# Kernel optimization log

Measured on AMD Instinct MI355X. Metric: run time of the kernel, lower is better.

## Reference

```python
import jax, jax.numpy as jnp
import numpy as np
from math import sqrt

D_MODEL = 768
N_HEADS = 12
D_K = 64
D_V = 64
LN_EPS = 1e-5
NEG = -1e9


def layer_norm(x, g, b):
    mu = jnp.mean(x, axis=-1, keepdims=True)
    var = jnp.mean((x - mu) ** 2, axis=-1, keepdims=True)
    return (x - mu) * jax.lax.rsqrt(var + LN_EPS) * g + b


def setup_inputs() -> dict:
    key = jax.random.key(0)
    ks = jax.random.split(key, 8)
    B, S = 4, 1024
    pro1 = jax.random.normal(ks[0], (B, S, D_MODEL), dtype=jnp.float32)
    pro2 = jax.random.normal(ks[1], (B, S, D_MODEL), dtype=jnp.float32)
    # attn_mask is [B, H, S2, S1]; transpose(2,3) masks scores [B,H,S1,S2]
    mask1_2 = jax.random.bernoulli(ks[2], 0.3, (B, N_HEADS, S, S))
    sc = 1.0 / np.sqrt(D_MODEL)
    W_Q = jax.random.normal(ks[3], (D_MODEL, D_K * N_HEADS), dtype=jnp.float32) * sc
    W_K = jax.random.normal(ks[4], (D_MODEL, D_K * N_HEADS), dtype=jnp.float32) * sc
    fc1 = jax.random.normal(ks[5], (D_V * N_HEADS, D_MODEL), dtype=jnp.float32) * sc
    g1 = jnp.ones((D_MODEL,), jnp.float32)
    b1 = jnp.zeros((D_MODEL,), jnp.float32)
    g2 = jnp.ones((D_MODEL,), jnp.float32)
    b2 = jnp.zeros((D_MODEL,), jnp.float32)
    return {"pro1": pro1, "pro2": pro2, "mask1_2": mask1_2,
            "W_Q": W_Q, "W_K": W_K, "fc1": fc1,
            "g1": g1, "b1": b1, "g2": g2, "b2": b2}


def reference(pro1, pro2, mask1_2, W_Q, W_K, fc1, g1, b1, g2, b2):
    B, S1, _ = pro1.shape
    S2 = pro2.shape[1]
    # project and split heads: [B, H, S, d_k]
    Q = (pro1 @ W_Q).reshape(B, S1, N_HEADS, D_K).transpose(0, 2, 1, 3)
    K = (pro2 @ W_K).reshape(B, S2, N_HEADS, D_K).transpose(0, 2, 1, 3)
    scores = jnp.einsum('bhsd,bhtd->bhst', Q, K) / sqrt(D_K)  # [B,H,S1,S2]
    mask = jnp.swapaxes(mask1_2, 2, 3)  # attn_mask.transpose(2,3)
    scores = jnp.where(mask, NEG, scores)
    attn1 = jax.nn.softmax(scores, axis=-1)                  # over S2
    attn2 = jax.nn.softmax(jnp.swapaxes(scores, -1, -2), axis=-1)  # over S1
    ctx1 = jnp.einsum('bhst,bhtd->bhsd', attn1, K)  # [B,H,S1,d_k]
    ctx2 = jnp.einsum('bhts,bhsd->bhtd', attn2, Q)  # [B,H,S2,d_k]
    c1 = ctx1.transpose(0, 2, 1, 3).reshape(B, S1, N_HEADS * D_V)
    c2 = ctx2.transpose(0, 2, 1, 3).reshape(B, S2, N_HEADS * D_V)
    # NOTE: original applies fc1 to BOTH branches (fc2 is dead code)
    o1 = layer_norm(c1 @ fc1, g1, b1)
    o2 = layer_norm(c2 @ fc1, g2, b2)
    return (o1, o2)
```

## Files before the change

### kernel.cpp

```cpp
#include <hip/hip_runtime.h>
#include <hip/hip_bf16.h>
#include <stdint.h>

#define S 1024
#define DMODEL 768
#define NH 12
#define DK 64
#define BB 4
#define BH 48
#define M4 4096

typedef __attribute__((ext_vector_type(8))) short bf16x8;
typedef __attribute__((ext_vector_type(4))) float f32x4;
typedef __attribute__((ext_vector_type(4))) _Float16 f16x4;
typedef __attribute__((ext_vector_type(8))) _Float16 f16x8;

static __device__ __forceinline__ unsigned short f2bf(float f) {
  unsigned int u = __float_as_uint(f);
  unsigned int r = u + 0x7FFFu + ((u >> 16) & 1u);
  return (unsigned short)(r >> 16);
}
static __device__ __forceinline__ bf16x8 ldfrag(const unsigned short* p) {
  uint4 q = *reinterpret_cast<const uint4*>(p);
  return __builtin_bit_cast(bf16x8, q);
}
static __device__ __forceinline__ f16x8 ldfragh(const unsigned short* p) {
  uint4 q = *reinterpret_cast<const uint4*>(p);
  return __builtin_bit_cast(f16x8, q);
}
static __device__ __forceinline__ unsigned short h2u(_Float16 h) {
  return __builtin_bit_cast(unsigned short, h);
}
static __device__ __forceinline__ void gl2lds16(const unsigned short* g, unsigned short* l) {
  __builtin_amdgcn_global_load_lds(
      (const __attribute__((address_space(1))) unsigned int*)g,
      (__attribute__((address_space(3))) unsigned int*)l, 16, 0, 0);
}

__global__ __launch_bounds__(256) void k_convert(const float* __restrict__ in,
                                                 unsigned short* __restrict__ out, int n4) {
  int i = blockIdx.x * 256 + threadIdx.x;
  if (i < n4) {
    float4 v = reinterpret_cast<const float4*>(in)[i];
    ushort4 o;
    o.x = f2bf(v.x); o.y = f2bf(v.y); o.z = f2bf(v.z); o.w = f2bf(v.w);
    reinterpret_cast<ushort4*>(out)[i] = o;
  }
}

__global__ __launch_bounds__(256) void k_transpose(const float* w0, const float* w1, const float* w2,
                                                   unsigned short* o0, unsigned short* o1, unsigned short* o2) {
  const float* in = blockIdx.z == 0 ? w0 : (blockIdx.z == 1 ? w1 : w2);
  unsigned short* out = blockIdx.z == 0 ? o0 : (blockIdx.z == 1 ? o1 : o2);
  __shared__ float tile[32][33];
  int n0 = blockIdx.x * 32, k0 = blockIdx.y * 32;
  int tid = threadIdx.x;
  int r = tid >> 3, c = (tid & 7) * 4;
  float4 v = *reinterpret_cast<const float4*>(in + (size_t)(k0 + r) * DMODEL + n0 + c);
  tile[r][c] = v.x; tile[r][c + 1] = v.y; tile[r][c + 2] = v.z; tile[r][c + 3] = v.w;
  __syncthreads();
  ushort4 o;
  o.x = f2bf(tile[c + 0][r]);
  o.y = f2bf(tile[c + 1][r]);
  o.z = f2bf(tile[c + 2][r]);
  o.w = f2bf(tile[c + 3][r]);
  *reinterpret_cast<ushort4*>(out + (size_t)(n0 + r) * DMODEL + k0 + c) = o;
}

__global__ __launch_bounds__(256) void k_pack(const int* __restrict__ mask,
                                              unsigned int* __restrict__ mp2) {
  int bh = blockIdx.y;
  int w = threadIdx.x >> 6, lane = threadIdx.x & 63;
  int tile = blockIdx.x * 4 + w;
  int ti = tile >> 4, tj = tile & 15;
  int t0 = ti * 64, s0 = tj * 64;
  const int* mb = mask + (size_t)bh * S * S;
  unsigned long long rowword = 0;
#pragma unroll 8
  for (int r = 0; r < 64; ++r) {
    int v = mb[(size_t)(t0 + r) * S + s0 + lane];
    unsigned long long b = __ballot(v != 0);
    if (lane == r) rowword = b;
  }
  unsigned int* p2 = mp2 + (size_t)bh * 32 * S;
  p2[((s0 >> 5) + 0) * S + t0 + lane] = (unsigned int)rowword;
  p2[((s0 >> 5) + 1) * S + t0 + lane] = (unsigned int)(rowword >> 32);
}

__global__ __launch_bounds__(256, 3) void k_gemm(
    int mode,
    const unsigned short* __restrict__ A0, const unsigned short* __restrict__ A1,
    const unsigned short* __restrict__ Bt0, const unsigned short* __restrict__ Bt1,
    unsigned short* __restrict__ oQ0, unsigned short* __restrict__ oQ1,
    unsigned short* __restrict__ oT0, unsigned short* __restrict__ oT1,
    float* __restrict__ oF0, float* __restrict__ oF1) {
  const unsigned short* A = blockIdx.z ? A1 : A0;
  const unsigned short* Bt = blockIdx.z ? Bt1 : Bt0;
  __shared__ __align__(16) unsigned short As[128 * 64];
  __shared__ __align__(16) unsigned short Bs[128 * 64];
  int tid = threadIdx.x;
  int m0 = blockIdx.x * 128, n0 = blockIdx.y * 128;
  int w = tid >> 6, lane = tid & 63, lane15 = lane & 15, quad = lane >> 4;
  int row0 = (w >> 1) * 64, col0 = (w & 1) * 64;
  f32x4 acc[4][4] = {};

  const unsigned short* gA[4];
  const unsigned short* gB[4];
  unsigned short* lA[4];
  unsigned short* lB[4];
  {
    int lr = lane >> 3;
    int ch = lane & 7;
#pragma unroll
    for (int i = 0; i < 4; ++i) {
      int r = w * 32 + i * 8 + lr;
      int cs = ((ch ^ (r & 7)) * 8);
      gA[i] = A + (size_t)(m0 + r) * DMODEL + cs;
      gB[i] = Bt + (size_t)(n0 + r) * DMODEL + cs;
      lA[i] = &As[(w * 32 + i * 8) * 64];
      lB[i] = &Bs[(w * 32 + i * 8) * 64];
    }
  }
  int l7 = lane15 & 7;
#pragma unroll
  for (int i = 0; i < 4; ++i) { gl2lds16(gA[i], lA[i]); gl2lds16(gB[i], lB[i]); }

  for (int kc = 0; kc < 12; ++kc) {
    __syncthreads();
#pragma unroll
    for (int ks = 0; ks < 2; ++ks) {
      int co = (((ks * 4 + quad) ^ l7) * 8);
      bf16x8 a[4], b[4];
#pragma unroll
      for (int i = 0; i < 4; ++i) a[i] = ldfrag(&As[(row0 + i * 16 + lane15) * 64 + co]);
#pragma unroll
      for (int j = 0; j < 4; ++j) b[j] = ldfrag(&Bs[(col0 + j * 16 + lane15) * 64 + co]);
#pragma unroll
      for (int i = 0; i < 4; ++i)
#pragma unroll
        for (int j = 0; j < 4; ++j)
          acc[i][j] = __builtin_amdgcn_mfma_f32_16x16x32_bf16(a[i], b[j], acc[i][j], 0, 0, 0);
    }
    __syncthreads();
    if (kc < 11) {
      int ko = (kc + 1) * 64;
#pragma unroll
      for (int i = 0; i < 4; ++i) { gl2lds16(gA[i] + ko, lA[i]); gl2lds16(gB[i] + ko, lB[i]); }
    }
  }

  if (mode == 0) {
    unsigned short* out = blockIdx.z ? oQ1 : oQ0;
    unsigned short* outT = blockIdx.z ? oT1 : oT0;
    f16x4 iden;
#pragma unroll
    for (int i = 0; i < 4; ++i) iden[i] = (_Float16)((quad * 4 + i) == lane15 ? 1.0f : 0.0f);
    f32x4 zero4 = {};
#pragma unroll
    for (int i = 0; i < 4; ++i)
#pragma unroll
      for (int j = 0; j < 4; ++j) {
        f16x4 cf;
#pragma unroll
        for (int reg = 0; reg < 4; ++reg) cf[reg] = (_Float16)acc[i][j][reg];
        f32x4 tq = __builtin_amdgcn_mfma_f32_16x16x16f16(cf, iden, zero4, 0, 0, 0);
        {
          int m = m0 + row0 + i * 16 + lane15;
          int n = n0 + col0 + j * 16 + quad * 4;
          int b = m >> 10, s = m & 1023, h = n >> 6, d = n & 63;
          ushort4 o;
          o.x = h2u((_Float16)tq[0]); o.y = h2u((_Float16)tq[1]);
          o.z = h2u((_Float16)tq[2]); o.w = h2u((_Float16)tq[3]);
          *reinterpret_cast<ushort4*>(&out[(((size_t)(b * NH + h)) * S + s) * DK + d]) = o;
        }
        {
          int n = n0 + col0 + j * 16 + lane15;
          int m = m0 + row0 + i * 16 + quad * 4;
          int b = m >> 10, s = m & 1023, h = n >> 6, d = n & 63;
          ushort4 o;
          o.x = h2u((_Float16)acc[i][j][0]); o.y = h2u((_Float16)acc[i][j][1]);
          o.z = h2u((_Float16)acc[i][j][2]); o.w = h2u((_Float16)acc[i][j][3]);
          *reinterpret_cast<ushort4*>(&outT[(((size_t)(b * NH + h)) * DK + d) * S + s]) = o;
        }
      }
  } else {
    float* out = blockIdx.z ? oF1 : oF0;
#pragma unroll
    for (int i = 0; i < 4; ++i)
#pragma unroll
      for (int j = 0; j < 4; ++j)
#pragma unroll
        for (int reg = 0; reg < 4; ++reg) {
          int m = m0 + row0 + i * 16 + quad * 4 + reg;
          int n = n0 + col0 + j * 16 + lane15;
          out[(size_t)m * DMODEL + n] = acc[i][j][reg];
        }
  }
}

__global__ __launch_bounds__(256, 3) void k_attn(
    const unsigned short* __restrict__ Qb, const unsigned short* __restrict__ Kb,
    const unsigned short* __restrict__ QT, const unsigned short* __restrict__ KT,
    const unsigned int* __restrict__ mp2,
    unsigned short* __restrict__ c1, unsigned short* __restrict__ c2) {
  int bh = blockIdx.y, path = blockIdx.z;
  int s0b = blockIdx.x * 128;
  const unsigned short* X = path ? Kb : Qb;
  const unsigned short* Y = path ? Qb : Kb;
  const unsigned short* YT = path ? QT : KT;
  unsigned short* outc = path ? c2 : c1;

  __shared__ __align__(16) unsigned short YS[64 * 72];
  __shared__ __align__(16) unsigned short YTS[64 * 72];
  __shared__ unsigned int MWS[256];

  const unsigned short* Xb = X + (size_t)bh * S * DK;
  const unsigned short* Yb = Y + (size_t)bh * S * DK;
  const unsigned short* YTb = YT + (size_t)bh * DK * S;
  const unsigned int* mbg = mp2 + (size_t)bh * 32 * S;

  int tid = threadIdx.x;
  int w = tid >> 6, lane = tid & 63, lane15 = lane & 15, quad = lane >> 4;
  int s0w = s0b + w * 32;

  f16x8 xf[2][2];
#pragma unroll
  for (int rg = 0; rg < 2; ++rg) {
    xf[rg][0] = ldfragh(Xb + (size_t)(s0w + rg * 16 + lane15) * DK + quad * 8);
    xf[rg][1] = ldfragh(Xb + (size_t)(s0w + rg * 16 + lane15) * DK + 32 + quad * 8);
  }

  int sr4 = tid >> 2, sc4 = (tid & 3) * 16;
  const unsigned short* gY = Yb + (size_t)sr4 * DK + sc4;
  const unsigned short* gYT = YTb + (size_t)sr4 * S + sc4;
  uint4 y0 = *reinterpret_cast<const uint4*>(gY);
  uint4 y1 = *reinterpret_cast<const uint4*>(gY + 8);
  uint4 t0 = *reinterpret_cast<const uint4*>(gYT);
  uint4 t1 = *reinterpret_cast<const uint4*>(gYT + 8);
  int mws_idx = (path == 0) ? ((tid & 63) * 4 + (tid >> 6)) : ((tid & 127) * 2 + (tid >> 7));
  unsigned int mwv = (path == 0)
      ? mbg[((size_t)((s0b >> 5) + (tid >> 6))) * S + (tid & 63)]
      : mbg[((size_t)(tid >> 7)) * S + s0b + (tid & 127)];

  f32x4 outa[2][4] = {};
  float lsum[2] = {0.f, 0.f};

  for (int jc = 0; jc < 16; ++jc) {
    __syncthreads();
    *reinterpret_cast<uint4*>(&YS[sr4 * 72 + sc4]) = y0;
    *reinterpret_cast<uint4*>(&YS[sr4 * 72 + sc4 + 8]) = y1;
    *reinterpret_cast<uint4*>(&YTS[sr4 * 72 + sc4]) = t0;
    *reinterpret_cast<uint4*>(&YTS[sr4 * 72 + sc4 + 8]) = t1;
    MWS[mws_idx] = mwv;
    {
      int jn = (jc + 1 < 16) ? (jc + 1) * 64 : jc * 64;
      y0 = *reinterpret_cast<const uint4*>(gY + (size_t)jn * DK);
      y1 = *reinterpret_cast<const uint4*>(gY + (size_t)jn * DK + 8);
      t0 = *reinterpret_cast<const uint4*>(gYT + jn);
      t1 = *reinterpret_cast<const uint4*>(gYT + jn + 8);
      mwv = (path == 0)
          ? mbg[((size_t)((s0b >> 5) + (tid >> 6))) * S + jn + (tid & 63)]
          : mbg[((size_t)((jn >> 5) + (tid >> 7))) * S + s0b + (tid & 127)];
    }
    __syncthreads();

    f32x4 scv[4][2];
#pragma unroll
    for (int st = 0; st < 4; ++st) {
      f16x8 a0 = ldfragh(&YS[(st * 16 + lane15) * 72 + quad * 8]);
      f16x8 a1 = ldfragh(&YS[(st * 16 + lane15) * 72 + 32 + quad * 8]);
#pragma unroll
      for (int rg = 0; rg < 2; ++rg) {
        f32x4 v = {};
        v = __builtin_amdgcn_mfma_f32_16x16x32_f16(a0, xf[rg][0], v, 0, 0, 0);
        v = __builtin_amdgcn_mfma_f32_16x16x32_f16(a1, xf[rg][1], v, 0, 0, 0);
        scv[st][rg] = v;
      }
    }
    f16x4 pfa[4][2];
    if (path == 0) {
#pragma unroll
      for (int st = 0; st < 4; ++st)
#pragma unroll
        for (int reg = 0; reg < 4; ++reg) {
          unsigned int wdv = MWS[(st * 16 + quad * 4 + reg) * 4 + w];
#pragma unroll
          for (int rg = 0; rg < 2; ++rg) {
            float e = __expf(scv[st][rg][reg] * 0.125f);
            float p = ((wdv >> (unsigned)(rg * 16 + lane15)) & 1u) ? 0.f : e;
            lsum[rg] += p;
            pfa[st][rg][reg] = (_Float16)p;
          }
        }
    } else {
#pragma unroll
      for (int rg = 0; rg < 2; ++rg) {
        unsigned int wv0 = MWS[(w * 32 + rg * 16 + lane15) * 2 + 0];
        unsigned int wv1 = MWS[(w * 32 + rg * 16 + lane15) * 2 + 1];
#pragma unroll
        for (int st = 0; st < 4; ++st) {
          unsigned int wdv = (st < 2) ? wv0 : wv1;
#pragma unroll
          for (int reg = 0; reg < 4; ++reg) {
            unsigned int sh = (unsigned)((st & 1) * 16 + quad * 4 + reg);
            float e = __expf(scv[st][rg][reg] * 0.125f);
            float p = ((wdv >> sh) & 1u) ? 0.f : e;
            lsum[rg] += p;
            pfa[st][rg][reg] = (_Float16)p;
          }
        }
      }
    }
#pragma unroll
    for (int st = 0; st < 4; ++st)
#pragma unroll
      for (int dsub = 0; dsub < 4; ++dsub) {
        uint2 q = *reinterpret_cast<const uint2*>(&YTS[(dsub * 16 + lane15) * 72 + st * 16 + quad * 4]);
        f16x4 yb = __builtin_bit_cast(f16x4, q);
#pragma unroll
        for (int rg = 0; rg < 2; ++rg)
          outa[rg][dsub] = __builtin_amdgcn_mfma_f32_16x16x16f16(pfa[st][rg], yb, outa[rg][dsub], 0, 0, 0);
      }
  }

#pragma unroll
  for (int rg = 0; rg < 2; ++rg) {
    lsum[rg] += __shfl_xor(lsum[rg], 16);
    lsum[rg] += __shfl_xor(lsum[rg], 32);
  }
  float rinv[2][4];
#pragma unroll
  for (int rg = 0; rg < 2; ++rg)
#pragma unroll
    for (int reg = 0; reg < 4; ++reg)
      rinv[rg][reg] = 1.0f / __shfl(lsum[rg], quad * 4 + reg);

  int b = bh / NH, h = bh % NH;
#pragma unroll
  for (int rg = 0; rg < 2; ++rg)
#pragma unroll
    for (int dsub = 0; dsub < 4; ++dsub)
#pragma unroll
      for (int reg = 0; reg < 4; ++reg) {
        float v = outa[rg][dsub][reg] * rinv[rg][reg];
        int srow = s0w + rg * 16 + quad * 4 + reg;
        size_t idx = ((size_t)(b * S) + srow) * DMODEL + h * DK + dsub * 16 + lane15;
        outc[idx] = f2bf(v);
      }
}

__global__ __launch_bounds__(256) void k_ln(const float* __restrict__ f1, const float* __restrict__ f2,
                                            const float* __restrict__ g1, const float* __restrict__ b1,
                                            const float* __restrict__ g2, const float* __restrict__ b2,
                                            float* __restrict__ out) {
  int rowg = blockIdx.x;
  int sel = rowg >> 12;
  int row = rowg & 4095;
  const float* in = sel ? f2 : f1;
  const float* g = sel ? g2 : g1;
  const float* be = sel ? b2 : b1;
  int tid = threadIdx.x;
  const float* p = in + (size_t)row * DMODEL;
  float x0 = p[tid], x1 = p[tid + 256], x2 = p[tid + 512];
  float s = x0 + x1 + x2;
  float ss = x0 * x0 + x1 * x1 + x2 * x2;
#pragma unroll
  for (int m = 1; m < 64; m <<= 1) { s += __shfl_xor(s, m); ss += __shfl_xor(ss, m); }
  __shared__ float ps[4], pss[4];
  int w = tid >> 6;
  if ((tid & 63) == 0) { ps[w] = s; pss[w] = ss; }
  __syncthreads();
  s = ps[0] + ps[1] + ps[2] + ps[3];
  ss = pss[0] + pss[1] + pss[2] + pss[3];
  float mu = s * (1.0f / 768.0f);
  float var = ss * (1.0f / 768.0f) - mu * mu;
  float rstd = rsqrtf(var + 1e-5f);
  float* o = out + ((size_t)sel * M4 + row) * DMODEL;
  o[tid] = (x0 - mu) * rstd * g[tid] + be[tid];
  o[tid + 256] = (x1 - mu) * rstd * g[tid + 256] + be[tid + 256];
  o[tid + 512] = (x2 - mu) * rstd * g[tid + 512] + be[tid + 512];
}

extern "C" void kernel_launch(void* const* d_in, const int* in_sizes, int n_in,
                              void* d_out, int out_size, void* d_ws, size_t ws_size,
                              hipStream_t stream) {
  const float* pro1 = (const float*)d_in[0];
  const float* pro2 = (const float*)d_in[1];
  const int* mask = (const int*)d_in[2];
  const float* WQ = (const float*)d_in[3];
  const float* WK = (const float*)d_in[4];
  const float* FC1 = (const float*)d_in[5];
  const float* g1 = (const float*)d_in[6];
  const float* b1 = (const float*)d_in[7];
  const float* g2 = (const float*)d_in[8];
  const float* b2 = (const float*)d_in[9];
  float* out = (float*)d_out;
  char* ws = (char*)d_ws;

  unsigned short* pro1b = (unsigned short*)(ws + 0);
  unsigned short* pro2b = (unsigned short*)(ws + 6291456);
  float* f1 = (float*)(ws + 0);
  unsigned short* wqt = (unsigned short*)(ws + 12582912);
  unsigned short* wkt = (unsigned short*)(ws + 13762560);
  unsigned short* fc1t = (unsigned short*)(ws + 14942208);
  unsigned short* Qb = (unsigned short*)(ws + 16121856);
  unsigned short* Kb = (unsigned short*)(ws + 22413312);
  unsigned short* QT = (unsigned short*)(ws + 28704768);
  unsigned short* KT = (unsigned short*)(ws + 34996224);
  unsigned int* mp2 = (unsigned int*)(ws + 41287680);
  float* f2 = (float*)(ws + 47579136);
  unsigned short* c1 = (unsigned short*)(ws + 60162048);
  unsigned short* c2 = (unsigned short*)(ws + 66453504);

  k_convert<<<3072, 256, 0, stream>>>(pro1, pro1b, 786432);
  k_convert<<<3072, 256, 0, stream>>>(pro2, pro2b, 786432);
  k_transpose<<<dim3(24, 24, 3), 256, 0, stream>>>(WQ, WK, FC1, wqt, wkt, fc1t);
  k_pack<<<dim3(64, BH), 256, 0, stream>>>(mask, mp2);
  k_gemm<<<dim3(32, 6, 2), 256, 0, stream>>>(0, pro1b, pro2b, wqt, wkt,
                                             Qb, Kb, QT, KT, nullptr, nullptr);
  k_attn<<<dim3(8, BH, 2), 256, 0, stream>>>(Qb, Kb, QT, KT, mp2, c1, c2);
  k_gemm<<<dim3(32, 6, 2), 256, 0, stream>>>(1, c1, c2, fc1t, fc1t,
                                             nullptr, nullptr, nullptr, nullptr, f1, f2);
  k_ln<<<8192, 256, 0, stream>>>(f1, f2, g1, b1, g2, b2, out);
}
```

Baseline: 415.6 us.

## Double-buffer attention tiles with direct global-to-LDS loads and XOR swizzle

The attention kernel now double-buffers the Y and Y-transpose tiles in shared memory. They are filled with direct global-to-LDS loads, one barrier per iteration, and an XOR-swizzled layout replaces the padded one. Mask words are kept in registers and broadcast with lane shuffles instead of being staged through shared memory. The 1/sqrt(d_k) scale is folded into the Q projection epilogue, which removes a multiply per score. The cost is more LDS per block and a reliance on the async-load ordering being correct with a single barrier.

Result: no change. 419.8 us (+1.0%).

```diff
diff --git a/kernel.cpp b/kernel.cpp
--- a/kernel.cpp
+++ b/kernel.cpp
@@ -152,6 +152,7 @@
   if (mode == 0) {
     unsigned short* out = blockIdx.z ? oQ1 : oQ0;
     unsigned short* outT = blockIdx.z ? oT1 : oT0;
+    float qs = blockIdx.z ? 1.0f : 0.125f;
     f16x4 iden;
 #pragma unroll
     for (int i = 0; i < 4; ++i) iden[i] = (_Float16)((quad * 4 + i) == lane15 ? 1.0f : 0.0f);
@@ -162,7 +163,7 @@
       for (int j = 0; j < 4; ++j) {
         f16x4 cf;
 #pragma unroll
-        for (int reg = 0; reg < 4; ++reg) cf[reg] = (_Float16)acc[i][j][reg];
+        for (int reg = 0; reg < 4; ++reg) cf[reg] = (_Float16)(acc[i][j][reg] * qs);
         f32x4 tq = __builtin_amdgcn_mfma_f32_16x16x16f16(cf, iden, zero4, 0, 0, 0);
         {
           int m = m0 + row0 + i * 16 + lane15;
@@ -178,8 +179,8 @@
           int m = m0 + row0 + i * 16 + quad * 4;
           int b = m >> 10, s = m & 1023, h = n >> 6, d = n & 63;
           ushort4 o;
-          o.x = h2u((_Float16)acc[i][j][0]); o.y = h2u((_Float16)acc[i][j][1]);
-          o.z = h2u((_Float16)acc[i][j][2]); o.w = h2u((_Float16)acc[i][j][3]);
+          o.x = h2u((_Float16)(acc[i][j][0] * qs)); o.y = h2u((_Float16)(acc[i][j][1] * qs));
+          o.z = h2u((_Float16)(acc[i][j][2] * qs)); o.w = h2u((_Float16)(acc[i][j][3] * qs));
           *reinterpret_cast<ushort4*>(&outT[(((size_t)(b * NH + h)) * DK + d) * S + s]) = o;
         }
       }
@@ -210,9 +211,8 @@
   const unsigned short* YT = path ? QT : KT;
   unsigned short* outc = path ? c2 : c1;
 
-  __shared__ __align__(16) unsigned short YS[64 * 72];
-  __shared__ __align__(16) unsigned short YTS[64 * 72];
-  __shared__ unsigned int MWS[256];
+  __shared__ __align__(16) unsigned short YSb[2][64 * 64];
+  __shared__ __align__(16) unsigned short YTSb[2][64 * 64];
 
   const unsigned short* Xb = X + (size_t)bh * S * DK;
   const unsigned short* Yb = Y + (size_t)bh * S * DK;
@@ -230,45 +230,50 @@
     xf[rg][1] = ldfragh(Xb + (size_t)(s0w + rg * 16 + lane15) * DK + 32 + quad * 8);
   }
 
-  int sr4 = tid >> 2, sc4 = (tid & 3) * 16;
-  const unsigned short* gY = Yb + (size_t)sr4 * DK + sc4;
-  const unsigned short* gYT = YTb + (size_t)sr4 * S + sc4;
-  uint4 y0 = *reinterpret_cast<const uint4*>(gY);
-  uint4 y1 = *reinterpret_cast<const uint4*>(gY + 8);
-  uint4 t0 = *reinterpret_cast<const uint4*>(gYT);
-  uint4 t1 = *reinterpret_cast<const uint4*>(gYT + 8);
-  int mws_idx = (path == 0) ? ((tid & 63) * 4 + (tid >> 6)) : ((tid & 127) * 2 + (tid >> 7));
-  unsigned int mwv = (path == 0)
-      ? mbg[((size_t)((s0b >> 5) + (tid >> 6))) * S + (tid & 63)]
-      : mbg[((size_t)(tid >> 7)) * S + s0b + (tid & 127)];
+  const unsigned short* gYs[2];
+  const unsigned short* gTs[2];
+  int loff[2];
+  {
+    int lr = lane >> 3, lc = lane & 7;
+#pragma unroll
+    for (int i = 0; i < 2; ++i) {
+      int r = w * 16 + i * 8 + lr;
+      int cs = ((lc ^ (r & 7)) * 8);
+      gYs[i] = Yb + (size_t)r * DK + cs;
+      gTs[i] = YTb + (size_t)r * S + cs;
+      loff[i] = (w * 16 + i * 8) * 64;
+    }
+  }
+#pragma unroll
+  for (int i = 0; i < 2; ++i) { gl2lds16(gYs[i], &YSb[0][loff[i]]); gl2lds16(gTs[i], &YTSb[0][loff[i]]); }
+  unsigned int gw = (path == 0)
+      ? mbg[(size_t)((s0b >> 5) + w) * S + lane]
+      : mbg[(size_t)(lane >> 5) * S + s0b + w * 32 + (lane & 31)];
 
   f32x4 outa[2][4] = {};
   float lsum[2] = {0.f, 0.f};
 
   for (int jc = 0; jc < 16; ++jc) {
+    int p = jc & 1;
     __syncthreads();
-    *reinterpret_cast<uint4*>(&YS[sr4 * 72 + sc4]) = y0;
-    *reinterpret_cast<uint4*>(&YS[sr4 * 72 + sc4 + 8]) = y1;
-    *reinterpret_cast<uint4*>(&YTS[sr4 * 72 + sc4]) = t0;
-    *reinterpret_cast<uint4*>(&YTS[sr4 * 72 + sc4 + 8]) = t1;
-    MWS[mws_idx] = mwv;
-    {
-      int jn = (jc + 1 < 16) ? (jc + 1) * 64 : jc * 64;
-      y0 = *reinterpret_cast<const uint4*>(gY + (size_t)jn * DK);
-      y1 = *reinterpret_cast<const uint4*>(gY + (size_t)jn * DK + 8);
-      t0 = *reinterpret_cast<const uint4*>(gYT + jn);
-      t1 = *reinterpret_cast<const uint4*>(gYT + jn + 8);
-      mwv = (path == 0)
-          ? mbg[((size_t)((s0b >> 5) + (tid >> 6))) * S + jn + (tid & 63)]
-          : mbg[((size_t)((jn >> 5) + (tid >> 7))) * S + s0b + (tid & 127)];
-    }
-    __syncthreads();
+    if (jc < 15) {
+      size_t oy = (size_t)(jc + 1) * 64 * DK;
+      int ot = (jc + 1) * 64;
+#pragma unroll
+      for (int i = 0; i < 2; ++i) {
+        gl2lds16(gYs[i] + oy, &YSb[1 - p][loff[i]]);
+        gl2lds16(gTs[i] + ot, &YTSb[1 - p][loff[i]]);
+      }
+    }
+    const unsigned short* YS = YSb[p];
+    const unsigned short* YTS = YTSb[p];
 
     f32x4 scv[4][2];
 #pragma unroll
     for (int st = 0; st < 4; ++st) {
-      f16x8 a0 = ldfragh(&YS[(st * 16 + lane15) * 72 + quad * 8]);
-      f16x8 a1 = ldfragh(&YS[(st * 16 + lane15) * 72 + 32 + quad * 8]);
+      int row = st * 16 + lane15;
+      f16x8 a0 = ldfragh(&YS[row * 64 + ((quad ^ (row & 7)) * 8)]);
+      f16x8 a1 = ldfragh(&YS[row * 64 + (((4 + quad) ^ (row & 7)) * 8)]);
 #pragma unroll
       for (int rg = 0; rg < 2; ++rg) {
         f32x4 v = {};
@@ -283,39 +288,48 @@
       for (int st = 0; st < 4; ++st)
 #pragma unroll
         for (int reg = 0; reg < 4; ++reg) {
-          unsigned int wdv = MWS[(st * 16 + quad * 4 + reg) * 4 + w];
+          unsigned int wdv = __shfl(gw, st * 16 + quad * 4 + reg);
 #pragma unroll
           for (int rg = 0; rg < 2; ++rg) {
-            float e = __expf(scv[st][rg][reg] * 0.125f);
-            float p = ((wdv >> (unsigned)(rg * 16 + lane15)) & 1u) ? 0.f : e;
-            lsum[rg] += p;
-            pfa[st][rg][reg] = (_Float16)p;
+            float e = __expf(scv[st][rg][reg]);
+            float pp = ((wdv >> (unsigned)(rg * 16 + lane15)) & 1u) ? 0.f : e;
+            lsum[rg] += pp;
+            pfa[st][rg][reg] = (_Float16)pp;
           }
         }
     } else {
 #pragma unroll
       for (int rg = 0; rg < 2; ++rg) {
-        unsigned int wv0 = MWS[(w * 32 + rg * 16 + lane15) * 2 + 0];
-        unsigned int wv1 = MWS[(w * 32 + rg * 16 + lane15) * 2 + 1];
+        unsigned int wv0 = __shfl(gw, rg * 16 + lane15);
+        unsigned int wv1 = __shfl(gw, 32 + rg * 16 + lane15);
 #pragma unroll
         for (int st = 0; st < 4; ++st) {
           unsigned int wdv = (st < 2) ? wv0 : wv1;
 #pragma unroll
           for (int reg = 0; reg < 4; ++reg) {
             unsigned int sh = (unsigned)((st & 1) * 16 + quad * 4 + reg);
-            float e = __expf(scv[st][rg][reg] * 0.125f);
-            float p = ((wdv >> sh) & 1u) ? 0.f : e;
-            lsum[rg] += p;
-            pfa[st][rg][reg] = (_Float16)p;
+            float e = __expf(scv[st][rg][reg]);
+            float pp = ((wdv >> sh) & 1u) ? 0.f : e;
+            lsum[rg] += pp;
+            pfa[st][rg][reg] = (_Float16)pp;
           }
         }
       }
     }
+    if (jc < 15) {
+      int jn = (jc + 1) * 64;
+      gw = (path == 0)
+          ? mbg[(size_t)((s0b >> 5) + w) * S + jn + lane]
+          : mbg[(size_t)((jn >> 5) + (lane >> 5)) * S + s0b + w * 32 + (lane & 31)];
+    }
 #pragma unroll
     for (int st = 0; st < 4; ++st)
 #pragma unroll
       for (int dsub = 0; dsub < 4; ++dsub) {
-        uint2 q = *reinterpret_cast<const uint2*>(&YTS[(dsub * 16 + lane15) * 72 + st * 16 + quad * 4]);
+        int d = dsub * 16 + lane15;
+        int c0 = st * 2 + (quad >> 1);
+        uint2 q = *reinterpret_cast<const uint2*>(
+            &YTS[d * 64 + ((c0 ^ (d & 7)) * 8) + (quad & 1) * 4]);
         f16x4 yb = __builtin_bit_cast(f16x4, q);
 #pragma unroll
         for (int rg = 0; rg < 2; ++rg)
```
